# Performance work log

Measured on AMD Instinct MI355X. Metric: run time of the kernel, lower is better.

## Reference

```python
import jax, jax.numpy as jnp
import numpy as np


def setup_inputs() -> dict:
    key = jax.random.key(0)
    k1, k2 = jax.random.split(key)
    qs = jax.random.normal(k1, (64, 32, 128), dtype=jnp.float32)   # (n_queries, n_query_tokens, dim)
    ps = jax.random.normal(k2, (64, 1024, 128), dtype=jnp.float32)  # (n_docs, n_doc_tokens, dim)
    return {"qs": qs, "ps": ps}


def reference(qs, ps):
    # ColBERT MaxSim: for each (query b, doc c), sum over query tokens of the
    # max similarity against all doc tokens.
    # scores[b,c,n,s] = sum_d qs[b,n,d] * ps[c,s,d]
    sim = jnp.einsum('bnd,csd->bcns', qs, ps)  # (n_q, n_d, tok_q, tok_d)
    scores = sim.max(axis=3).sum(axis=2)       # (n_q, n_d)
    return scores
```

## Files before the change

kernel.cpp:

```cpp
#include <hip/hip_runtime.h>
#include <stdint.h>


typedef __bf16 bf16x8 __attribute__((ext_vector_type(8)));
typedef float floatx16 __attribute__((ext_vector_type(16)));

__device__ inline bf16x8 cvt8(const float4& a, const float4& b) {
  bf16x8 r;
  r[0] = (__bf16)a.x; r[1] = (__bf16)a.y; r[2] = (__bf16)a.z; r[3] = (__bf16)a.w;
  r[4] = (__bf16)b.x; r[5] = (__bf16)b.y; r[6] = (__bf16)b.z; r[7] = (__bf16)b.w;
  return r;
}

__device__ inline float rmax16(const floatx16& a) {
  float m0 = fmaxf(fmaxf(a[0], a[1]), fmaxf(a[2], a[3]));
  float m1 = fmaxf(fmaxf(a[4], a[5]), fmaxf(a[6], a[7]));
  float m2 = fmaxf(fmaxf(a[8], a[9]), fmaxf(a[10], a[11]));
  float m3 = fmaxf(fmaxf(a[12], a[13]), fmaxf(a[14], a[15]));
  return fmaxf(fmaxf(m0, m1), fmaxf(m2, m3));
}

#define ZERO16 {0, 0, 0, 0, 0, 0, 0, 0, 0, 0, 0, 0, 0, 0, 0, 0}

__global__ __launch_bounds__(256) void maxsim_kernel(const float* __restrict__ qs,
                                                     const float* __restrict__ ps,
                                                     float* __restrict__ out) {
  const int lane = threadIdx.x & 63;
  const int wave = threadIdx.x >> 6;

  const int xcd = blockIdx.x & 7;
  const int slot = blockIdx.x >> 3;
  const int c = xcd * 8 + (slot >> 3);
  const int bg = slot & 7;
  const int qb0 = bg * 8 + wave * 2;

  const int row = lane & 31;
  const int hi8 = (lane >> 5) * 8;

  bf16x8 qf[2][8];
#pragma unroll
  for (int bb = 0; bb < 2; ++bb) {
    const float* q = qs + ((qb0 + bb) * 32 + row) * 128 + hi8;
#pragma unroll
    for (int k = 0; k < 8; ++k) {
      float4 a = *(const float4*)(q + k * 16);
      float4 b = *(const float4*)(q + k * 16 + 4);
      qf[bb][k] = cvt8(a, b);
    }
  }

  __shared__ __align__(16) ushort lds_p[2][4096];

  const float* pg = ps + (c * 1024 + row) * 128 + hi8;

#pragma unroll
  for (int jj = 0; jj < 2; ++jj) {
    const int j = wave * 2 + jj;
    const float* src = pg + j * 16;
    float4 a = *(const float4*)src;
    float4 b = *(const float4*)(src + 4);
    *(bf16x8*)(&lds_p[0][j * 512 + lane * 8]) = cvt8(a, b);
  }
  __syncthreads();

  float vmax0 = -3.4e38f, vmax1 = -3.4e38f;
  int cb = 0;

#pragma unroll 1
  for (int t = 0; t < 32; ++t) {
    float4 Fa0, Fb0, Fa1, Fb1;
    if (t < 31) {
      const float* src = pg + (t + 1) * 32 * 128 + (wave * 2) * 16;
      Fa0 = *(const float4*)src;
      Fb0 = *(const float4*)(src + 4);
      Fa1 = *(const float4*)(src + 16);
      Fb1 = *(const float4*)(src + 20);
    }
    const ushort* lp = &lds_p[cb][0] + lane * 8;
    floatx16 acc0 = ZERO16, acc1 = ZERO16;
#pragma unroll
    for (int k = 0; k < 8; ++k) {
      bf16x8 af = *(const bf16x8*)(lp + k * 512);
      acc0 = __builtin_amdgcn_mfma_f32_32x32x16_bf16(af, qf[0][k], acc0, 0, 0, 0);
      acc1 = __builtin_amdgcn_mfma_f32_32x32x16_bf16(af, qf[1][k], acc1, 0, 0, 0);
    }
    vmax0 = fmaxf(vmax0, rmax16(acc0));
    vmax1 = fmaxf(vmax1, rmax16(acc1));
    if (t < 31) {
      ushort* dst = &lds_p[cb ^ 1][(wave * 2) * 512 + lane * 8];
      *(bf16x8*)dst = cvt8(Fa0, Fb0);
      *(bf16x8*)(dst + 512) = cvt8(Fa1, Fb1);
    }
    __syncthreads();
    cb ^= 1;
  }

  vmax0 = fmaxf(vmax0, __shfl_xor(vmax0, 32, 64));
  vmax1 = fmaxf(vmax1, __shfl_xor(vmax1, 32, 64));
#pragma unroll
  for (int o = 16; o > 0; o >>= 1) {
    vmax0 += __shfl_xor(vmax0, o, 64);
    vmax1 += __shfl_xor(vmax1, o, 64);
  }
  if (lane == 0) {
    out[(qb0 + 0) * 64 + c] = vmax0;
    out[(qb0 + 1) * 64 + c] = vmax1;
  }
}

extern "C" void kernel_launch(void* const* d_in, const int* in_sizes, int n_in,
                              void* d_out, int out_size, void* d_ws, size_t ws_size,
                              hipStream_t stream) {
  const float* qs = (const float*)d_in[0];
  const float* ps = (const float*)d_in[1];
  float* out = (float*)d_out;
  (void)d_ws; (void)ws_size;

  maxsim_kernel<<<dim3(512), dim3(256), 0, stream>>>(qs, ps, out);
}
```

Measured before the change: 124.5 us.

## Stream doc tiles via direct global-to-LDS loads with triple buffering

Replaces register-staged loads (global to VGPR, convert to bf16, store to LDS) with global_load_lds DMA of raw fp32 into a three-stage LDS ring, prefetching two tiles ahead. Explicit vmcnt waits and raw barriers replace __syncthreads. The fp32-to-bf16 conversion moves to after the LDS read, so every wave converts each tile redundantly. LDS traffic and footprint double because the ring now holds fp32, in exchange for deeper prefetch and less register pressure.

```diff
diff --git a/kernel.cpp b/kernel.cpp
--- a/kernel.cpp
+++ b/kernel.cpp
@@ -18,6 +18,12 @@
   float m2 = fmaxf(fmaxf(a[8], a[9]), fmaxf(a[10], a[11]));
   float m3 = fmaxf(fmaxf(a[12], a[13]), fmaxf(a[14], a[15]));
   return fmaxf(fmaxf(m0, m1), fmaxf(m2, m3));
+}
+
+typedef __attribute__((address_space(1))) const void gas_t;
+typedef __attribute__((address_space(3))) void las_t;
+__device__ inline void gload_lds16f(const float* g, float* l) {
+  __builtin_amdgcn_global_load_lds((gas_t*)g, (las_t*)l, 16, 0, 0);
 }
 
 #define ZERO16 {0, 0, 0, 0, 0, 0, 0, 0, 0, 0, 0, 0, 0, 0, 0, 0}
@@ -49,50 +55,53 @@
     }
   }
 
-  __shared__ __align__(16) ushort lds_p[2][4096];
+  __shared__ __align__(16) float lds_p[3][4096];
 
-  const float* pg = ps + (c * 1024 + row) * 128 + hi8;
+  const int pg_lane = (c * 1024 + row) * 128 + hi8;
 
-#pragma unroll
-  for (int jj = 0; jj < 2; ++jj) {
-    const int j = wave * 2 + jj;
-    const float* src = pg + j * 16;
-    float4 a = *(const float4*)src;
-    float4 b = *(const float4*)(src + 4);
-    *(bf16x8*)(&lds_p[0][j * 512 + lane * 8]) = cvt8(a, b);
+#define STAGE(L, tt)                                                          \
+  _Pragma("unroll") for (int jj = 0; jj < 4; ++jj) {                          \
+    const int m = wave * 4 + jj;                                              \
+    const int j = m >> 1, h = m & 1;                                          \
+    gload_lds16f(ps + pg_lane + (tt) * 4096 + j * 16 + h * 4,                 \
+                 (L) + m * 256);                                              \
   }
-  __syncthreads();
+
+  float* pA = &lds_p[0][0];
+  float* pB = &lds_p[1][0];
+  float* pC = &lds_p[2][0];
+
+  STAGE(pA, 0)
+  STAGE(pB, 1)
+  asm volatile("s_waitcnt vmcnt(4)" ::: "memory");
+  __builtin_amdgcn_s_barrier();
 
   float vmax0 = -3.4e38f, vmax1 = -3.4e38f;
-  int cb = 0;
 
 #pragma unroll 1
   for (int t = 0; t < 32; ++t) {
-    float4 Fa0, Fb0, Fa1, Fb1;
-    if (t < 31) {
-      const float* src = pg + (t + 1) * 32 * 128 + (wave * 2) * 16;
-      Fa0 = *(const float4*)src;
-      Fb0 = *(const float4*)(src + 4);
-      Fa1 = *(const float4*)(src + 16);
-      Fb1 = *(const float4*)(src + 20);
+    if (t + 2 < 32) {
+      STAGE(pC, t + 2)
     }
-    const ushort* lp = &lds_p[cb][0] + lane * 8;
+    const float* lp = pA + lane * 4;
     floatx16 acc0 = ZERO16, acc1 = ZERO16;
 #pragma unroll
     for (int k = 0; k < 8; ++k) {
-      bf16x8 af = *(const bf16x8*)(lp + k * 512);
+      float4 lo = *(const float4*)(lp + (2 * k) * 256);
+      float4 hi = *(const float4*)(lp + (2 * k + 1) * 256);
+      bf16x8 af = cvt8(lo, hi);
       acc0 = __builtin_amdgcn_mfma_f32_32x32x16_bf16(af, qf[0][k], acc0, 0, 0, 0);
       acc1 = __builtin_amdgcn_mfma_f32_32x32x16_bf16(af, qf[1][k], acc1, 0, 0, 0);
     }
     vmax0 = fmaxf(vmax0, rmax16(acc0));
     vmax1 = fmaxf(vmax1, rmax16(acc1));
-    if (t < 31) {
-      ushort* dst = &lds_p[cb ^ 1][(wave * 2) * 512 + lane * 8];
-      *(bf16x8*)dst = cvt8(Fa0, Fb0);
-      *(bf16x8*)(dst + 512) = cvt8(Fa1, Fb1);
+    if (t + 2 < 32) {
+      asm volatile("s_waitcnt vmcnt(4)" ::: "memory");
+    } else if (t + 1 < 32) {
+      asm volatile("s_waitcnt vmcnt(0)" ::: "memory");
     }
-    __syncthreads();
-    cb ^= 1;
+    if (t + 1 < 32) __builtin_amdgcn_s_barrier();
+    float* tmp = pA; pA = pB; pB = pC; pC = tmp;
   }
 
   vmax0 = fmaxf(vmax0, __shfl_xor(vmax0, 32, 64));
```

Result: slower. 128.1 us (+2.9%).
